# Kernel optimization log

Hardware: AMD Instinct MI355X
Metric: run time of the kernel (lower is better)

## Reference

```python
import jax, jax.numpy as jnp
import numpy as np

GROUPS = 8


def setup_inputs() -> dict:
    key = jax.random.key(0)
    k1, k2, k3 = jax.random.split(key, 3)
    B, H, W, Cin, Cout, KH, KW = 32, 56, 56, 256, 256, 3, 3
    inputs = jax.random.normal(k1, (B, H, W, Cin), dtype=jnp.float32)
    # HWIO kernel for grouped conv: input channel dim = Cin // groups
    fan_in = KH * KW * (Cin // GROUPS)
    limit = np.sqrt(6.0 / (fan_in + Cout // GROUPS))  # glorot-ish scale
    kernel = jax.random.uniform(k2, (KH, KW, Cin // GROUPS, Cout), dtype=jnp.float32,
                                minval=-limit, maxval=limit)
    bias = jnp.zeros((Cout,), dtype=jnp.float32)
    return {"inputs": inputs, "kernel": kernel, "bias": bias}


def reference(inputs, kernel, bias):
    # Equivalent to per-group slice + Conv2D + concat: a single grouped conv.
    # inputs: [B,H,W,Cin] NHWC; kernel: [KH,KW,Cin//G,Cout] HWIO
    out = jax.lax.conv_general_dilated(
        inputs, kernel,
        window_strides=(1, 1),
        padding="SAME",
        lhs_dilation=(1, 1),
        rhs_dilation=(1, 1),
        dimension_numbers=("NHWC", "HWIO", "NHWC"),
        feature_group_count=GROUPS,
    )
    out = out + bias  # broadcast over [B,H,W,Cout]
    return out
```

## Files before the change

### kernel.cpp

```cpp
#include <hip/hip_runtime.h>


#define TPW 7

typedef __bf16 bf16x8 __attribute__((ext_vector_type(8)));
typedef float floatx4 __attribute__((ext_vector_type(4)));
typedef unsigned short ushortx8 __attribute__((ext_vector_type(8)));

__device__ __forceinline__ unsigned short f2bf(float f) {
    unsigned int u = __builtin_bit_cast(unsigned int, f);
    u += 0x7fffu + ((u >> 16) & 1u);
    return (unsigned short)(u >> 16);
}

__global__ __launch_bounds__(256)
void wprep(const float* __restrict__ wgt, unsigned short* __restrict__ wbf) {
    const int i = blockIdx.x * 256 + threadIdx.x;
    const int co256 = i & 255;
    const int tmp   = i >> 8;
    const int ci    = tmp & 31;
    const int kk    = tmp >> 5;
    const int g  = co256 >> 5;
    const int co = co256 & 31;
    wbf[((g * 9 + kk) * 32 + co) * 32 + ci] = f2bf(wgt[i]);
}

__global__ __launch_bounds__(256, 4)
void gconv_mfma(const float* __restrict__ in, const unsigned short* __restrict__ wbf,
                const float* __restrict__ bias, float* __restrict__ out) {
    const int g  = blockIdx.x;
    const int rt = blockIdx.y;
    const int b  = blockIdx.z;
    const int y0 = rt * 8;

    __shared__ unsigned short lds_in[10 * 58 * 32];

    const int tid = threadIdx.x;

    float4 lo[10], hi[10];
    int ldsoff[10];
#pragma unroll
    for (int i = 0; i < 10; ++i) {
        const int gidx = tid + i * 256;
        const bool valid = gidx < 2320;
        const int sub = gidx & 3;
        const int cr  = gidx >> 2;
        const int col = cr % 58;
        const int row = cr / 58;
        const int gy = y0 - 1 + row;
        const int gx = col - 1;
        ldsoff[i] = valid ? (row * 58 + col) * 32 + sub * 8 : -1;
        lo[i] = make_float4(0.f, 0.f, 0.f, 0.f);
        hi[i] = make_float4(0.f, 0.f, 0.f, 0.f);
        if (valid && (unsigned)gy < 56u && (unsigned)gx < 56u) {
            const float* p = &in[(((b * 56 + gy) * 56 + gx) * 256) + g * 32 + sub * 8];
            lo[i] = *reinterpret_cast<const float4*>(p);
            hi[i] = *reinterpret_cast<const float4*>(p + 4);
        }
    }
#pragma unroll
    for (int i = 0; i < 10; ++i) {
        if (ldsoff[i] >= 0) {
            ushortx8 pk;
            pk[0] = f2bf(lo[i].x); pk[1] = f2bf(lo[i].y);
            pk[2] = f2bf(lo[i].z); pk[3] = f2bf(lo[i].w);
            pk[4] = f2bf(hi[i].x); pk[5] = f2bf(hi[i].y);
            pk[6] = f2bf(hi[i].z); pk[7] = f2bf(hi[i].w);
            *reinterpret_cast<ushortx8*>(&lds_in[ldsoff[i]]) = pk;
        }
    }

    __syncthreads();

    const int wv   = tid >> 6;
    const int lane = tid & 63;
    const int lc   = lane & 15;
    const int quad = lane >> 4;

    int lane_base[TPW];
#pragma unroll
    for (int t = 0; t < TPW; ++t) {
        const int p  = (wv * TPW + t) * 16 + lc;
        const int yl = p / 56;
        const int xl = p - yl * 56;
        lane_base[t] = (yl * 58 + xl) * 32 + quad * 8;
    }

    const unsigned short* wq = &wbf[((g * 9) * 32) * 32 + quad * 8];

    floatx4 acc[TPW][2];
#pragma unroll
    for (int t = 0; t < TPW; ++t) {
        acc[t][0] = (floatx4)(0.f);
        acc[t][1] = (floatx4)(0.f);
    }

    bf16x8 b0 = *reinterpret_cast<const bf16x8*>(&wq[(0 * 32 + lc) * 32]);
    bf16x8 b1 = *reinterpret_cast<const bf16x8*>(&wq[(0 * 32 + 16 + lc) * 32]);

#pragma unroll
    for (int kk = 0; kk < 9; ++kk) {
        const int ky = kk / 3, kx = kk % 3;
        const int koff = (ky * 58 + kx) * 32;
        bf16x8 nb0 = b0, nb1 = b1;
        if (kk < 8) {
            nb0 = *reinterpret_cast<const bf16x8*>(&wq[((kk + 1) * 32 + lc) * 32]);
            nb1 = *reinterpret_cast<const bf16x8*>(&wq[((kk + 1) * 32 + 16 + lc) * 32]);
        }
#pragma unroll
        for (int t = 0; t < TPW; ++t) {
            const bf16x8 a = *reinterpret_cast<const bf16x8*>(&lds_in[lane_base[t] + koff]);
            acc[t][0] = __builtin_amdgcn_mfma_f32_16x16x32_bf16(a, b0, acc[t][0], 0, 0, 0);
            acc[t][1] = __builtin_amdgcn_mfma_f32_16x16x32_bf16(a, b1, acc[t][1], 0, 0, 0);
        }
        b0 = nb0; b1 = nb1;
    }

    __syncthreads();
    float* scr = reinterpret_cast<float*>(lds_in) + wv * 576;
    const float bv0 = bias[g * 32 + lc];
    const float bv1 = bias[g * 32 + 16 + lc];
    const int px_s = lane >> 2;
    const int c8   = (lane & 3) * 8;
#pragma unroll
    for (int t = 0; t < TPW; ++t) {
#pragma unroll
        for (int r = 0; r < 4; ++r) {
            const int px = quad * 4 + r;
            scr[px * 36 + lc]      = acc[t][0][r] + bv0;
            scr[px * 36 + 16 + lc] = acc[t][1][r] + bv1;
        }
        asm volatile("s_waitcnt lgkmcnt(0)" ::: "memory");
        const floatx4 oa = *reinterpret_cast<const floatx4*>(&scr[px_s * 36 + c8]);
        const floatx4 ob = *reinterpret_cast<const floatx4*>(&scr[px_s * 36 + c8 + 4]);
        const int p = (wv * TPW + t) * 16 + px_s;
        const int y = p / 56;
        const int x = p - y * 56;
        float* o = &out[(((b * 56) + y0 + y) * 56 + x) * 256 + g * 32 + c8];
        *reinterpret_cast<floatx4*>(o)     = oa;
        *reinterpret_cast<floatx4*>(o + 4) = ob;
        asm volatile("s_waitcnt lgkmcnt(0)" ::: "memory");
    }
}

__global__ __launch_bounds__(256, 2)
void gconv_mfma_ldsw(const float* __restrict__ in, const float* __restrict__ wgt,
                     const float* __restrict__ bias, float* __restrict__ out) {
    const int rt = blockIdx.y, g = blockIdx.x, b = blockIdx.z;
    const int y0 = rt * 8;
    __shared__ unsigned short lds_in[10 * 58 * 32];
    __shared__ unsigned short lds_w[9 * 32 * 32];
    const int tid = threadIdx.x;
    for (int i = tid; i < 9 * 32 * 32; i += 256) {
        const int co = i & 31, ci = (i >> 5) & 31, kk = i >> 10;
        lds_w[(kk * 32 + co) * 32 + ci] = f2bf(wgt[(kk * 32 + ci) * 256 + g * 32 + co]);
    }
    for (int c = tid; c < 10 * 58 * 8; c += 256) {
        const int row = c / 464, rem = c - row * 464, col = rem >> 3, q = rem & 7;
        const int gy = y0 - 1 + row, gx = col - 1;
        float4 v = make_float4(0.f, 0.f, 0.f, 0.f);
        if ((unsigned)gy < 56u && (unsigned)gx < 56u)
            v = *reinterpret_cast<const float4*>(&in[(((b * 56 + gy) * 56 + gx) * 256) + g * 32 + q * 4]);
        unsigned short p0 = f2bf(v.x), p1 = f2bf(v.y), p2 = f2bf(v.z), p3 = f2bf(v.w);
        unsigned short* d = &lds_in[(row * 58 + col) * 32 + q * 4];
        d[0] = p0; d[1] = p1; d[2] = p2; d[3] = p3;
    }
    __syncthreads();
    const int wv = tid >> 6, lane = tid & 63, lc = lane & 15, quad = lane >> 4;
    int lane_base[TPW];
#pragma unroll
    for (int t = 0; t < TPW; ++t) {
        const int p = (wv * TPW + t) * 16 + lc;
        const int yl = p / 56, xl = p - yl * 56;
        lane_base[t] = (yl * 58 + xl) * 32 + quad * 8;
    }
    floatx4 acc[TPW][2];
#pragma unroll
    for (int t = 0; t < TPW; ++t) { acc[t][0] = (floatx4)(0.f); acc[t][1] = (floatx4)(0.f); }
#pragma unroll
    for (int kk = 0; kk < 9; ++kk) {
        const int ky = kk / 3, kx = kk % 3;
        const int koff = (ky * 58 + kx) * 32;
        const bf16x8 bf0 = *reinterpret_cast<const bf16x8*>(&lds_w[(kk * 32 + lc) * 32 + quad * 8]);
        const bf16x8 bf1 = *reinterpret_cast<const bf16x8*>(&lds_w[(kk * 32 + 16 + lc) * 32 + quad * 8]);
#pragma unroll
        for (int t = 0; t < TPW; ++t) {
            const bf16x8 a = *reinterpret_cast<const bf16x8*>(&lds_in[lane_base[t] + koff]);
            acc[t][0] = __builtin_amdgcn_mfma_f32_16x16x32_bf16(a, bf0, acc[t][0], 0, 0, 0);
            acc[t][1] = __builtin_amdgcn_mfma_f32_16x16x32_bf16(a, bf1, acc[t][1], 0, 0, 0);
        }
    }
    const float bv0 = bias[g * 32 + lc], bv1 = bias[g * 32 + 16 + lc];
#pragma unroll
    for (int t = 0; t < TPW; ++t)
#pragma unroll
        for (int r = 0; r < 4; ++r) {
            const int p = (wv * TPW + t) * 16 + quad * 4 + r;
            const int y = p / 56, x = p - y * 56;
            float* o = &out[(((b * 56) + y0 + y) * 56 + x) * 256 + g * 32];
            o[lc] = acc[t][0][r] + bv0;
            o[16 + lc] = acc[t][1][r] + bv1;
        }
}

extern "C" void kernel_launch(void* const* d_in, const int* in_sizes, int n_in,
                              void* d_out, int out_size, void* d_ws, size_t ws_size,
                              hipStream_t stream) {
    const float* in   = (const float*)d_in[0];
    const float* wgt  = (const float*)d_in[1];
    const float* bias = (const float*)d_in[2];
    float* out        = (float*)d_out;
    dim3 grid(8, 7, 32);

    if (ws_size >= (size_t)(8 * 9 * 32 * 32 * sizeof(unsigned short))) {
        unsigned short* wbf = (unsigned short*)d_ws;
        wprep<<<dim3(288, 1, 1), dim3(256, 1, 1), 0, stream>>>(wgt, wbf);
        gconv_mfma<<<grid, dim3(256, 1, 1), 0, stream>>>(in, wbf, bias, out);
    } else {
        gconv_mfma_ldsw<<<grid, dim3(256, 1, 1), 0, stream>>>(in, wgt, bias, out);
    }
}
```

Before: 202.5 us.

## Stage input tile via direct global-to-LDS loads before bf16 conversion

Replaces the register-staged input load with global_load_lds direct-to-LDS 16-byte transfers of the fp32 halo tile, using clamped addresses. Each thread then reads the fp32 values back from LDS, converts them to bf16 (zeroing padding pixels) and writes them in place. The goal is to cut register pressure and VGPR round-trips on the load path. In exchange it doubles LDS use to fp32 size and drops occupancy to 2 blocks per SM, and it adds extra barriers and an LDS read/write pass.

New measurement: 199.5 us. Within noise of the previous version (-1.5%).

```diff
diff --git a/kernel.cpp b/kernel.cpp
--- a/kernel.cpp
+++ b/kernel.cpp
@@ -5,7 +5,10 @@
 
 typedef __bf16 bf16x8 __attribute__((ext_vector_type(8)));
 typedef float floatx4 __attribute__((ext_vector_type(4)));
-typedef unsigned short ushortx8 __attribute__((ext_vector_type(8)));
+typedef unsigned short ushortx4 __attribute__((ext_vector_type(4)));
+
+typedef const __attribute__((address_space(1))) void* gas_ptr;
+typedef __attribute__((address_space(3))) void* las_ptr;
 
 __device__ __forceinline__ unsigned short f2bf(float f) {
     unsigned int u = __builtin_bit_cast(unsigned int, f);
@@ -25,7 +28,7 @@
     wbf[((g * 9 + kk) * 32 + co) * 32 + ci] = f2bf(wgt[i]);
 }
 
-__global__ __launch_bounds__(256, 4)
+__global__ __launch_bounds__(256, 2)
 void gconv_mfma(const float* __restrict__ in, const unsigned short* __restrict__ wbf,
                 const float* __restrict__ bias, float* __restrict__ out) {
     const int g  = blockIdx.x;
@@ -33,43 +36,53 @@
     const int b  = blockIdx.z;
     const int y0 = rt * 8;
 
-    __shared__ unsigned short lds_in[10 * 58 * 32];
+    __shared__ float lds_f32[10 * 58 * 32];
+    unsigned short* lds_in = reinterpret_cast<unsigned short*>(lds_f32);
 
     const int tid = threadIdx.x;
 
-    float4 lo[10], hi[10];
-    int ldsoff[10];
-#pragma unroll
-    for (int i = 0; i < 10; ++i) {
-        const int gidx = tid + i * 256;
-        const bool valid = gidx < 2320;
-        const int sub = gidx & 3;
-        const int cr  = gidx >> 2;
-        const int col = cr % 58;
-        const int row = cr / 58;
-        const int gy = y0 - 1 + row;
-        const int gx = col - 1;
-        ldsoff[i] = valid ? (row * 58 + col) * 32 + sub * 8 : -1;
-        lo[i] = make_float4(0.f, 0.f, 0.f, 0.f);
-        hi[i] = make_float4(0.f, 0.f, 0.f, 0.f);
-        if (valid && (unsigned)gy < 56u && (unsigned)gx < 56u) {
-            const float* p = &in[(((b * 56 + gy) * 56 + gx) * 256) + g * 32 + sub * 8];
-            lo[i] = *reinterpret_cast<const float4*>(p);
-            hi[i] = *reinterpret_cast<const float4*>(p + 4);
-        }
-    }
-#pragma unroll
-    for (int i = 0; i < 10; ++i) {
-        if (ldsoff[i] >= 0) {
-            ushortx8 pk;
-            pk[0] = f2bf(lo[i].x); pk[1] = f2bf(lo[i].y);
-            pk[2] = f2bf(lo[i].z); pk[3] = f2bf(lo[i].w);
-            pk[4] = f2bf(hi[i].x); pk[5] = f2bf(hi[i].y);
-            pk[6] = f2bf(hi[i].z); pk[7] = f2bf(hi[i].w);
-            *reinterpret_cast<ushortx8*>(&lds_in[ldsoff[i]]) = pk;
-        }
-    }
-
+#pragma unroll
+    for (int r = 0; r < 19; ++r) {
+        const int c = tid + r * 256;
+        if (c < 4640) {
+            const int px  = c >> 3;
+            const int sub = c & 7;
+            const int row = px / 58;
+            const int col = px - row * 58;
+            int gy = y0 - 1 + row;  gy = gy < 0 ? 0 : (gy > 55 ? 55 : gy);
+            int gx = col - 1;       gx = gx < 0 ? 0 : (gx > 55 ? 55 : gx);
+            const float* gp = &in[(((b * 56 + gy) * 56 + gx) * 256) + g * 32 + sub * 4];
+            __builtin_amdgcn_global_load_lds((gas_ptr)gp, (las_ptr)&lds_f32[c * 4], 16, 0, 0);
+        }
+    }
+    __syncthreads();
+
+    floatx4 v[19];
+#pragma unroll
+    for (int r = 0; r < 19; ++r) {
+        const int c = tid + r * 256;
+        if (c < 4640) v[r] = *reinterpret_cast<const floatx4*>(&lds_f32[c * 4]);
+    }
+    __syncthreads();
+
+#pragma unroll
+    for (int r = 0; r < 19; ++r) {
+        const int c = tid + r * 256;
+        if (c < 4640) {
+            const int px  = c >> 3;
+            const int row = px / 58;
+            const int col = px - row * 58;
+            const int gy = y0 - 1 + row;
+            const int gx = col - 1;
+            const bool ok = ((unsigned)gy < 56u) && ((unsigned)gx < 56u);
+            ushortx4 p;
+            p[0] = ok ? f2bf(v[r][0]) : (unsigned short)0;
+            p[1] = ok ? f2bf(v[r][1]) : (unsigned short)0;
+            p[2] = ok ? f2bf(v[r][2]) : (unsigned short)0;
+            p[3] = ok ? f2bf(v[r][3]) : (unsigned short)0;
+            *reinterpret_cast<ushortx4*>(&lds_in[c * 4]) = p;
+        }
+    }
     __syncthreads();
 
     const int wv   = tid >> 6;
@@ -117,7 +130,7 @@
     }
 
     __syncthreads();
-    float* scr = reinterpret_cast<float*>(lds_in) + wv * 576;
+    float* scr = lds_f32 + wv * 576;
     const float bv0 = bias[g * 32 + lc];
     const float bv1 = bias[g * 32 + 16 + lc];
     const int px_s = lane >> 2;
```
